# Kernel tuning notes

Hardware: AMD Instinct MI355X
Metric: run time of the kernel (lower is better)

The kernel has to match this reference:

```python
import jax, jax.numpy as jnp
import numpy as np

THETA = 0.5
NEG_SLOPE = 0.2


def setup_inputs() -> dict:
    key = jax.random.key(0)
    k1, k2, k3, k4, k5 = jax.random.split(key, 5)
    B, N, K, E, F = 32, 50000, 32, 6, 3
    return {
        "x": jax.random.normal(k1, (B, N), dtype=jnp.float32),
        "node_embeddings": jax.random.normal(k2, (N, E), dtype=jnp.float32),
        "fc_weight": jax.random.normal(k3, (F, E), dtype=jnp.float32),
        "fc_bias": jax.random.normal(k4, (F,), dtype=jnp.float32),
        "neighbor_list": jax.random.randint(k5, (N, K), 0, N, dtype=jnp.int32),
    }


def reference(x, node_embeddings, fc_weight, fc_bias, neighbor_list):
    # e: (B, N, E) = broadcast-add of scalar feature x and node embeddings
    e = x[..., None] + node_embeddings[None, :, :]
    # f: (B, N, F) = LeakyReLU(e @ W^T + b)
    f = jax.nn.leaky_relu(jnp.einsum('bne,fe->bnf', e, fc_weight) + fc_bias,
                          negative_slope=NEG_SLOPE)
    # gather neighbor features: (B, N, K, F); negative indices wrap like torch
    f_nbr = f[:, neighbor_list]
    df = f[:, :, None, :] - f_nbr               # (B, N, K, F)
    w = jnp.exp(-(df * df).sum(-1) / (2.0 * THETA)).mean(0)  # (N, K)
    mask = (neighbor_list >= 0).astype(w.dtype)
    return w * mask
```

## Files before the change

### kernel.cpp

```cpp
#include <hip/hip_runtime.h>

#define NN 50000
#define BB 32
#define KK 32
#define TN 64
#define GN 8

typedef __attribute__((ext_vector_type(2))) _Float16 half2_t;
typedef __attribute__((ext_vector_type(4))) _Float16 half4_t;
typedef __attribute__((ext_vector_type(8))) _Float16 half8_t;

__device__ __forceinline__ half4_t g_dup0(half8_t v) {
    return __builtin_shufflevector(v, v, 0, 1, 0, 1);
}
__device__ __forceinline__ half4_t g_dup1(half8_t v) {
    return __builtin_shufflevector(v, v, 2, 3, 2, 3);
}
__device__ __forceinline__ half4_t g_dup2(half8_t v) {
    return __builtin_shufflevector(v, v, 4, 5, 4, 5);
}

__global__ __launch_bounds__(256) void prep_kernel(
    const float* __restrict__ x,
    const float* __restrict__ emb,
    const float* __restrict__ W,
    const float* __restrict__ bias,
    half2_t* __restrict__ xT,
    half8_t* __restrict__ gh)
{
    __shared__ float xs[BB][TN + 1];

    const int n0 = blockIdx.x * TN;
    const int t  = threadIdx.x;

#pragma unroll
    for (int j = 0; j < 8; ++j) {
        int idx = j * 256 + t;
        int r = idx >> 6, c = idx & 63;
        int n = n0 + c;
        xs[r][c] = (n < NN) ? x[r * NN + n] : 0.f;
    }
    __syncthreads();

#pragma unroll
    for (int it = 0; it < 4; ++it) {
        int slot = it * 256 + t;
        int nl = slot >> 4, b2 = slot & 15;
        int n = n0 + nl;
        if (n < NN) {
            half2_t p;
            p.x = (_Float16)xs[2 * b2][nl];
            p.y = (_Float16)xs[2 * b2 + 1][nl];
            xT[n * 16 + b2] = p;
            if (b2 == 0) {
                float e[6];
#pragma unroll
                for (int q = 0; q < 6; ++q) e[q] = emb[n * 6 + q];
                half8_t gv;
#pragma unroll
                for (int j = 0; j < 3; ++j) {
                    float s = bias[j];
#pragma unroll
                    for (int q = 0; q < 6; ++q) s += e[q] * W[j * 6 + q];
                    gv[2 * j] = (_Float16)s;
                    gv[2 * j + 1] = (_Float16)s;
                }
                gv[6] = (_Float16)0.f; gv[7] = (_Float16)0.f;
                gh[n] = gv;
            }
        }
    }
}

__global__ __launch_bounds__(256) void gather_kernel(
    const half4_t* __restrict__ xT4,
    const half8_t* __restrict__ gh,
    const float* __restrict__ W,
    const int* __restrict__ nbr,
    float* __restrict__ out)
{
    __shared__ int nbr_sh[GN * KK];

    const int t  = threadIdx.x;
    const int n0 = blockIdx.x * GN;

    nbr_sh[t] = nbr[n0 * KK + t];
    __syncthreads();

    half4_t ws4[3];
#pragma unroll
    for (int j = 0; j < 3; ++j) {
        float s = 0.f;
#pragma unroll
        for (int q = 0; q < 6; ++q) s += W[j * 6 + q];
        _Float16 h = (_Float16)s;
        ws4[j].x = h; ws4[j].y = h; ws4[j].z = h; ws4[j].w = h;
    }
    half4_t lk;
    lk.x = (_Float16)0.2f; lk.y = (_Float16)0.2f;
    lk.z = (_Float16)0.2f; lk.w = (_Float16)0.2f;

    const int l  = t & 7;
    const int sg = t >> 3;
    const int nl = sg >> 2;
    const int kg = (sg & 3) * 8;
    const int n  = n0 + nl;

    half4_t xn4 = xT4[n * 8 + l];
    half8_t gn8 = gh[n];
    half4_t fn[3];
    {
        half4_t u0 = xn4 * ws4[0] + g_dup0(gn8);
        fn[0] = __builtin_elementwise_max(u0, u0 * lk);
        half4_t u1 = xn4 * ws4[1] + g_dup1(gn8);
        fn[1] = __builtin_elementwise_max(u1, u1 * lk);
        half4_t u2 = xn4 * ws4[2] + g_dup2(gn8);
        fn[2] = __builtin_elementwise_max(u2, u2 * lk);
    }

    const int mbase = nl * KK + kg;

#pragma unroll
    for (int i = 0; i < 8; ++i) {
        int m  = nbr_sh[mbase + i];
        int mc = m > 0 ? m : 0;
        half4_t xm4 = xT4[mc * 8 + l];
        half8_t gm8 = gh[mc];

        half4_t acc;
        acc.x = (_Float16)0.f; acc.y = (_Float16)0.f;
        acc.z = (_Float16)0.f; acc.w = (_Float16)0.f;
        {
            half4_t u, d;
            u = xm4 * ws4[0] + g_dup0(gm8);
            u = __builtin_elementwise_max(u, u * lk);
            d = fn[0] - u; acc = d * d + acc;
            u = xm4 * ws4[1] + g_dup1(gm8);
            u = __builtin_elementwise_max(u, u * lk);
            d = fn[1] - u; acc = d * d + acc;
            u = xm4 * ws4[2] + g_dup2(gm8);
            u = __builtin_elementwise_max(u, u * lk);
            d = fn[2] - u; acc = d * d + acc;
        }
        float v = (__expf(-(float)acc.x) + __expf(-(float)acc.y))
                + (__expf(-(float)acc.z) + __expf(-(float)acc.w));
        v += __shfl_down(v, 4, 8);
        v += __shfl_down(v, 2, 8);
        v += __shfl_down(v, 1, 8);
        if (l == 0) out[n * KK + kg + i] = (m < 0) ? 0.f : v * (1.0f / 32.0f);
    }
}

extern "C" void kernel_launch(void* const* d_in, const int* in_sizes, int n_in,
                              void* d_out, int out_size, void* d_ws, size_t ws_size,
                              hipStream_t stream) {
    const float* x    = (const float*)d_in[0];
    const float* emb  = (const float*)d_in[1];
    const float* W    = (const float*)d_in[2];
    const float* bias = (const float*)d_in[3];
    const int*   nbr  = (const int*)d_in[4];
    float* out = (float*)d_out;

    half2_t* xT = (half2_t*)d_ws;
    half8_t* gh = (half8_t*)((char*)d_ws + NN * 16 * sizeof(half2_t));

    prep_kernel<<<(NN + TN - 1) / TN, 256, 0, stream>>>(x, emb, W, bias, xT, gh);
    gather_kernel<<<NN / GN, 256, 0, stream>>>((const half4_t*)xT, gh, W, nbr, out);
}
```

Baseline: 99.26 us.

## Widen gather lanes to half8, fold exp scale into weights, use exp2f

```diff
diff --git a/kernel.cpp b/kernel.cpp
--- a/kernel.cpp
+++ b/kernel.cpp
@@ -1,4 +1,5 @@
 #include <hip/hip_runtime.h>
+#include <math.h>
 
 #define NN 50000
 #define BB 32
@@ -6,18 +7,26 @@
 #define TN 64
 #define GN 8
 
+#define SCL 1.2011224087864498f
+
 typedef __attribute__((ext_vector_type(2))) _Float16 half2_t;
-typedef __attribute__((ext_vector_type(4))) _Float16 half4_t;
 typedef __attribute__((ext_vector_type(8))) _Float16 half8_t;
 
-__device__ __forceinline__ half4_t g_dup0(half8_t v) {
-    return __builtin_shufflevector(v, v, 0, 1, 0, 1);
+__device__ __forceinline__ half8_t dup0(half8_t v) {
+    return __builtin_shufflevector(v, v, 0, 1, 0, 1, 0, 1, 0, 1);
 }
-__device__ __forceinline__ half4_t g_dup1(half8_t v) {
-    return __builtin_shufflevector(v, v, 2, 3, 2, 3);
+__device__ __forceinline__ half8_t dup1(half8_t v) {
+    return __builtin_shufflevector(v, v, 2, 3, 2, 3, 2, 3, 2, 3);
 }
-__device__ __forceinline__ half4_t g_dup2(half8_t v) {
-    return __builtin_shufflevector(v, v, 4, 5, 4, 5);
+__device__ __forceinline__ half8_t dup2(half8_t v) {
+    return __builtin_shufflevector(v, v, 4, 5, 4, 5, 4, 5, 4, 5);
+}
+__device__ __forceinline__ half8_t splat8(float f) {
+    _Float16 h = (_Float16)f;
+    half8_t r;
+    r[0] = h; r[1] = h; r[2] = h; r[3] = h;
+    r[4] = h; r[5] = h; r[6] = h; r[7] = h;
+    return r;
 }
 
 __global__ __launch_bounds__(256) void prep_kernel(
@@ -62,6 +71,7 @@
                     float s = bias[j];
 #pragma unroll
                     for (int q = 0; q < 6; ++q) s += e[q] * W[j * 6 + q];
+                    s *= SCL;
                     gv[2 * j] = (_Float16)s;
                     gv[2 * j + 1] = (_Float16)s;
                 }
@@ -73,7 +83,7 @@
 }
 
 __global__ __launch_bounds__(256) void gather_kernel(
-    const half4_t* __restrict__ xT4,
+    const half8_t* __restrict__ xT8,
     const half8_t* __restrict__ gh,
     const float* __restrict__ W,
     const int* __restrict__ nbr,
@@ -87,67 +97,61 @@
     nbr_sh[t] = nbr[n0 * KK + t];
     __syncthreads();
 
-    half4_t ws4[3];
+    half8_t ws8[3];
 #pragma unroll
     for (int j = 0; j < 3; ++j) {
         float s = 0.f;
 #pragma unroll
         for (int q = 0; q < 6; ++q) s += W[j * 6 + q];
-        _Float16 h = (_Float16)s;
-        ws4[j].x = h; ws4[j].y = h; ws4[j].z = h; ws4[j].w = h;
+        ws8[j] = splat8(s * SCL);
     }
-    half4_t lk;
-    lk.x = (_Float16)0.2f; lk.y = (_Float16)0.2f;
-    lk.z = (_Float16)0.2f; lk.w = (_Float16)0.2f;
+    const half8_t lk = splat8(0.2f);
 
-    const int l  = t & 7;
-    const int sg = t >> 3;
-    const int nl = sg >> 2;
-    const int kg = (sg & 3) * 8;
+    const int l  = t & 3;
+    const int sg = t >> 2;
+    const int nl = sg >> 3;
+    const int kb = (sg & 7) * 4;
     const int n  = n0 + nl;
 
-    half4_t xn4 = xT4[n * 8 + l];
+    half8_t xn8 = xT8[n * 4 + l];
     half8_t gn8 = gh[n];
-    half4_t fn[3];
+    half8_t fn0, fn1, fn2;
     {
-        half4_t u0 = xn4 * ws4[0] + g_dup0(gn8);
-        fn[0] = __builtin_elementwise_max(u0, u0 * lk);
-        half4_t u1 = xn4 * ws4[1] + g_dup1(gn8);
-        fn[1] = __builtin_elementwise_max(u1, u1 * lk);
-        half4_t u2 = xn4 * ws4[2] + g_dup2(gn8);
-        fn[2] = __builtin_elementwise_max(u2, u2 * lk);
+        half8_t u;
+        u = xn8 * ws8[0] + dup0(gn8); fn0 = __builtin_elementwise_max(u, u * lk);
+        u = xn8 * ws8[1] + dup1(gn8); fn1 = __builtin_elementwise_max(u, u * lk);
+        u = xn8 * ws8[2] + dup2(gn8); fn2 = __builtin_elementwise_max(u, u * lk);
     }
 
-    const int mbase = nl * KK + kg;
+    const int mb = nl * KK + kb;
 
 #pragma unroll
-    for (int i = 0; i < 8; ++i) {
-        int m  = nbr_sh[mbase + i];
+    for (int i = 0; i < 4; ++i) {
+        int m  = nbr_sh[mb + i];
         int mc = m > 0 ? m : 0;
-        half4_t xm4 = xT4[mc * 8 + l];
+        half8_t xm8 = xT8[mc * 4 + l];
         half8_t gm8 = gh[mc];
 
-        half4_t acc;
-        acc.x = (_Float16)0.f; acc.y = (_Float16)0.f;
-        acc.z = (_Float16)0.f; acc.w = (_Float16)0.f;
+        half8_t acc = splat8(0.f);
         {
-            half4_t u, d;
-            u = xm4 * ws4[0] + g_dup0(gm8);
+            half8_t u, d;
+            u = xm8 * ws8[0] + dup0(gm8);
             u = __builtin_elementwise_max(u, u * lk);
-            d = fn[0] - u; acc = d * d + acc;
-            u = xm4 * ws4[1] + g_dup1(gm8);
+            d = fn0 - u; acc = d * d + acc;
+            u = xm8 * ws8[1] + dup1(gm8);
             u = __builtin_elementwise_max(u, u * lk);
-            d = fn[1] - u; acc = d * d + acc;
-            u = xm4 * ws4[2] + g_dup2(gm8);
+            d = fn1 - u; acc = d * d + acc;
+            u = xm8 * ws8[2] + dup2(gm8);
             u = __builtin_elementwise_max(u, u * lk);
-            d = fn[2] - u; acc = d * d + acc;
+            d = fn2 - u; acc = d * d + acc;
         }
-        float v = (__expf(-(float)acc.x) + __expf(-(float)acc.y))
-                + (__expf(-(float)acc.z) + __expf(-(float)acc.w));
-        v += __shfl_down(v, 4, 8);
-        v += __shfl_down(v, 2, 8);
-        v += __shfl_down(v, 1, 8);
-        if (l == 0) out[n * KK + kg + i] = (m < 0) ? 0.f : v * (1.0f / 32.0f);
+        float v = (exp2f(-(float)acc[0]) + exp2f(-(float)acc[1]))
+                + (exp2f(-(float)acc[2]) + exp2f(-(float)acc[3]))
+                + (exp2f(-(float)acc[4]) + exp2f(-(float)acc[5]))
+                + (exp2f(-(float)acc[6]) + exp2f(-(float)acc[7]));
+        v += __shfl_down(v, 2, 4);
+        v += __shfl_down(v, 1, 4);
+        if (l == 0) out[n * KK + kb + i] = (m < 0) ? 0.f : v * (1.0f / 32.0f);
     }
 }
 
@@ -165,5 +169,5 @@
     half8_t* gh = (half8_t*)((char*)d_ws + NN * 16 * sizeof(half2_t));
 
     prep_kernel<<<(NN + TN - 1) / TN, 256, 0, stream>>>(x, emb, W, bias, xT, gh);
-    gather_kernel<<<NN / GN, 256, 0, stream>>>((const half4_t*)xT, gh, W, nbr, out);
+    gather_kernel<<<NN / GN, 256, 0, stream>>>((const half8_t*)xT, gh, W, nbr, out);
 }
```

Result: no change. 101.2 us (+1.9%).

## Quantize x to 12-bit and pack per-node row into one 64-byte record

Applied to the files above, without the earlier changes.

```diff
diff --git a/kernel.cpp b/kernel.cpp
--- a/kernel.cpp
+++ b/kernel.cpp
@@ -1,4 +1,5 @@
 #include <hip/hip_runtime.h>
+#include <math.h>
 
 #define NN 50000
 #define BB 32
@@ -6,18 +7,40 @@
 #define TN 64
 #define GN 8
 
+#define SCL 1.2011224087864498f
+#define S0  (4096.0f / 12.0f)
+
 typedef __attribute__((ext_vector_type(2))) _Float16 half2_t;
 typedef __attribute__((ext_vector_type(4))) _Float16 half4_t;
-typedef __attribute__((ext_vector_type(8))) _Float16 half8_t;
-
-__device__ __forceinline__ half4_t g_dup0(half8_t v) {
-    return __builtin_shufflevector(v, v, 0, 1, 0, 1);
-}
-__device__ __forceinline__ half4_t g_dup1(half8_t v) {
-    return __builtin_shufflevector(v, v, 2, 3, 2, 3);
-}
-__device__ __forceinline__ half4_t g_dup2(half8_t v) {
-    return __builtin_shufflevector(v, v, 4, 5, 4, 5);
+
+
+__device__ __forceinline__ half2_t dupc(half4_t v, int which) {
+    if (which == 0) return __builtin_shufflevector(v, v, 0, 0);
+    if (which == 1) return __builtin_shufflevector(v, v, 1, 1);
+    return __builtin_shufflevector(v, v, 2, 2);
+}
+
+__device__ __forceinline__ half2_t pk2(float a, float b) {
+#if __has_builtin(__builtin_amdgcn_cvt_pkrtz)
+    return __builtin_bit_cast(half2_t, __builtin_amdgcn_cvt_pkrtz(a, b));
+#else
+    half2_t r; r.x = (_Float16)a; r.y = (_Float16)b; return r;
+#endif
+}
+
+__device__ __forceinline__ void unpack4(unsigned int lod, unsigned int hiw,
+                                        float K1, float K2,
+                                        half2_t& p01, half2_t& p23) {
+    unsigned int q0 = (lod & 0xFFu)         | ((hiw & 0x000Fu) << 8);
+    unsigned int q1 = ((lod >> 8) & 0xFFu)  | ((hiw & 0x00F0u) << 4);
+    unsigned int q2 = ((lod >> 16) & 0xFFu) | (((hiw >> 8) & 0xFu) << 8);
+    unsigned int q3 = (lod >> 24)           | (((hiw >> 12) & 0xFu) << 8);
+    float p0 = fmaf(__uint_as_float(0x46000000u | q0), K1, K2);
+    float p1 = fmaf(__uint_as_float(0x46000000u | q1), K1, K2);
+    float p2 = fmaf(__uint_as_float(0x46000000u | q2), K1, K2);
+    float p3 = fmaf(__uint_as_float(0x46000000u | q3), K1, K2);
+    p01 = pk2(p0, p1);
+    p23 = pk2(p2, p3);
 }
 
 __global__ __launch_bounds__(256) void prep_kernel(
@@ -25,10 +48,11 @@
     const float* __restrict__ emb,
     const float* __restrict__ W,
     const float* __restrict__ bias,
-    half2_t* __restrict__ xT,
-    half8_t* __restrict__ gh)
+    unsigned int* __restrict__ rows)
 {
     __shared__ float xs[BB][TN + 1];
+    __shared__ unsigned short qs[TN][BB];
+    __shared__ unsigned int ch[TN][2];
 
     const int n0 = blockIdx.x * TN;
     const int t  = threadIdx.x;
@@ -46,35 +70,61 @@
     for (int it = 0; it < 4; ++it) {
         int slot = it * 256 + t;
         int nl = slot >> 4, b2 = slot & 15;
+        int q0 = (int)rintf(xs[2 * b2][nl] * S0) + 2048;
+        int q1 = (int)rintf(xs[2 * b2 + 1][nl] * S0) + 2048;
+        q0 = q0 < 0 ? 0 : (q0 > 4095 ? 4095 : q0);
+        q1 = q1 < 0 ? 0 : (q1 > 4095 ? 4095 : q1);
+        qs[nl][2 * b2]     = (unsigned short)q0;
+        qs[nl][2 * b2 + 1] = (unsigned short)q1;
         int n = n0 + nl;
-        if (n < NN) {
-            half2_t p;
-            p.x = (_Float16)xs[2 * b2][nl];
-            p.y = (_Float16)xs[2 * b2 + 1][nl];
-            xT[n * 16 + b2] = p;
-            if (b2 == 0) {
-                float e[6];
-#pragma unroll
-                for (int q = 0; q < 6; ++q) e[q] = emb[n * 6 + q];
-                half8_t gv;
-#pragma unroll
-                for (int j = 0; j < 3; ++j) {
-                    float s = bias[j];
-#pragma unroll
-                    for (int q = 0; q < 6; ++q) s += e[q] * W[j * 6 + q];
-                    gv[2 * j] = (_Float16)s;
-                    gv[2 * j + 1] = (_Float16)s;
-                }
-                gv[6] = (_Float16)0.f; gv[7] = (_Float16)0.f;
-                gh[n] = gv;
+        if (b2 == 0 && n < NN) {
+            float e[6];
+#pragma unroll
+            for (int q = 0; q < 6; ++q) e[q] = emb[n * 6 + q];
+            unsigned short cb[3];
+#pragma unroll
+            for (int j = 0; j < 3; ++j) {
+                float s = bias[j];
+#pragma unroll
+                for (int q = 0; q < 6; ++q) s += e[q] * W[j * 6 + q];
+                _Float16 h = (_Float16)(s * SCL);
+                cb[j] = __builtin_bit_cast(unsigned short, h);
             }
-        }
+            ch[nl][0] = (unsigned int)cb[0] | ((unsigned int)cb[1] << 16);
+            ch[nl][1] = (unsigned int)cb[2];
+        }
+    }
+    __syncthreads();
+
+#pragma unroll
+    for (int it = 0; it < 4; ++it) {
+        int slot = it * 256 + t;
+        int nl = slot >> 4, d = slot & 15;
+        int n = n0 + nl;
+        if (n >= NN) continue;
+        unsigned int w = 0;
+        if (d < 8) {
+            int b = 4 * d;
+            w = ((unsigned int)(qs[nl][b] & 0xFF))
+              | ((unsigned int)(qs[nl][b + 1] & 0xFF) << 8)
+              | ((unsigned int)(qs[nl][b + 2] & 0xFF) << 16)
+              | ((unsigned int)(qs[nl][b + 3] & 0xFF) << 24);
+        } else if (d < 12) {
+            int i0 = 8 * (d - 8);
+#pragma unroll
+            for (int i = 0; i < 8; ++i)
+                w |= ((unsigned int)(qs[nl][i0 + i] >> 8)) << (4 * i);
+        } else if (d == 12) {
+            w = ch[nl][0];
+        } else if (d == 13) {
+            w = ch[nl][1];
+        }
+        rows[(size_t)n * 16 + d] = w;
     }
 }
 
 __global__ __launch_bounds__(256) void gather_kernel(
-    const half4_t* __restrict__ xT4,
-    const half8_t* __restrict__ gh,
+    const unsigned int* __restrict__ rows,
     const float* __restrict__ W,
     const int* __restrict__ nbr,
     float* __restrict__ out)
@@ -83,71 +133,82 @@
 
     const int t  = threadIdx.x;
     const int n0 = blockIdx.x * GN;
+    const unsigned short* rows16 = (const unsigned short*)rows;
 
     nbr_sh[t] = nbr[n0 * KK + t];
     __syncthreads();
 
-    half4_t ws4[3];
+    const float K1 = 1024.0f * SCL / S0;
+    const float K2 = -8390656.0f * SCL / S0;
+
+    half2_t wsh[3];
 #pragma unroll
     for (int j = 0; j < 3; ++j) {
         float s = 0.f;
 #pragma unroll
         for (int q = 0; q < 6; ++q) s += W[j * 6 + q];
         _Float16 h = (_Float16)s;
-        ws4[j].x = h; ws4[j].y = h; ws4[j].z = h; ws4[j].w = h;
-    }
-    half4_t lk;
-    lk.x = (_Float16)0.2f; lk.y = (_Float16)0.2f;
-    lk.z = (_Float16)0.2f; lk.w = (_Float16)0.2f;
+        wsh[j].x = h; wsh[j].y = h;
+    }
+    half2_t lk; lk.x = (_Float16)0.2f; lk.y = (_Float16)0.2f;
 
     const int l  = t & 7;
     const int sg = t >> 3;
     const int nl = sg >> 2;
-    const int kg = (sg & 3) * 8;
+    const int kb = (sg & 3) * 8;
     const int n  = n0 + nl;
 
-    half4_t xn4 = xT4[n * 8 + l];
-    half8_t gn8 = gh[n];
-    half4_t fn[3];
+    half2_t fn01[3], fn23[3];
     {
-        half4_t u0 = xn4 * ws4[0] + g_dup0(gn8);
-        fn[0] = __builtin_elementwise_max(u0, u0 * lk);
-        half4_t u1 = xn4 * ws4[1] + g_dup1(gn8);
-        fn[1] = __builtin_elementwise_max(u1, u1 * lk);
-        half4_t u2 = xn4 * ws4[2] + g_dup2(gn8);
-        fn[2] = __builtin_elementwise_max(u2, u2 * lk);
-    }
-
-    const int mbase = nl * KK + kg;
+        unsigned int lod = rows[(size_t)n * 16 + l];
+        unsigned short hiw = rows16[(size_t)n * 32 + 16 + l];
+        half4_t c4 = *(const half4_t*)(rows + (size_t)n * 16 + 12);
+        half2_t p01, p23;
+        unpack4(lod, hiw, K1, K2, p01, p23);
+#pragma unroll
+        for (int j = 0; j < 3; ++j) {
+            half2_t g = dupc(c4, j);
+            half2_t u = p01 * wsh[j] + g;
+            fn01[j] = __builtin_elementwise_max(u, u * lk);
+            u = p23 * wsh[j] + g;
+            fn23[j] = __builtin_elementwise_max(u, u * lk);
+        }
+    }
+
+    const int mb = nl * KK + kb;
 
 #pragma unroll
     for (int i = 0; i < 8; ++i) {
-        int m  = nbr_sh[mbase + i];
+        int m  = nbr_sh[mb + i];
         int mc = m > 0 ? m : 0;
-        half4_t xm4 = xT4[mc * 8 + l];
-        half8_t gm8 = gh[mc];
-
-        half4_t acc;
-        acc.x = (_Float16)0.f; acc.y = (_Float16)0.f;
-        acc.z = (_Float16)0.f; acc.w = (_Float16)0.f;
-        {
-            half4_t u, d;
-            u = xm4 * ws4[0] + g_dup0(gm8);
+        unsigned int lod = rows[(size_t)mc * 16 + l];
+        unsigned short hiw = rows16[(size_t)mc * 32 + 16 + l];
+        half4_t c4 = *(const half4_t*)(rows + (size_t)mc * 16 + 12);
+
+        half2_t p01, p23;
+        unpack4(lod, hiw, K1, K2, p01, p23);
+
+        half2_t a01, a23;
+        a01.x = (_Float16)0.f; a01.y = (_Float16)0.f;
+        a23 = a01;
+#pragma unroll
+        for (int j = 0; j < 3; ++j) {
+            half2_t g = dupc(c4, j);
+            half2_t u = p01 * wsh[j] + g;
             u = __builtin_elementwise_max(u, u * lk);
-            d = fn[0] - u; acc = d * d + acc;
-            u = xm4 * ws4[1] + g_dup1(gm8);
+            half2_t d = fn01[j] - u;
+            a01 = d * d + a01;
+            u = p23 * wsh[j] + g;
             u = __builtin_elementwise_max(u, u * lk);
-            d = fn[1] - u; acc = d * d + acc;
-            u = xm4 * ws4[2] + g_dup2(gm8);
-            u = __builtin_elementwise_max(u, u * lk);
-            d = fn[2] - u; acc = d * d + acc;
-        }
-        float v = (__expf(-(float)acc.x) + __expf(-(float)acc.y))
-                + (__expf(-(float)acc.z) + __expf(-(float)acc.w));
+            d = fn23[j] - u;
+            a23 = d * d + a23;
+        }
+        float v = (exp2f(-(float)a01.x) + exp2f(-(float)a01.y))
+                + (exp2f(-(float)a23.x) + exp2f(-(float)a23.y));
         v += __shfl_down(v, 4, 8);
         v += __shfl_down(v, 2, 8);
         v += __shfl_down(v, 1, 8);
-        if (l == 0) out[n * KK + kg + i] = (m < 0) ? 0.f : v * (1.0f / 32.0f);
+        if (l == 0) out[n * KK + kb + i] = (m < 0) ? 0.f : v * (1.0f / 32.0f);
     }
 }
 
@@ -161,9 +222,8 @@
     const int*   nbr  = (const int*)d_in[4];
     float* out = (float*)d_out;
 
-    half2_t* xT = (half2_t*)d_ws;
-    half8_t* gh = (half8_t*)((char*)d_ws + NN * 16 * sizeof(half2_t));
-
-    prep_kernel<<<(NN + TN - 1) / TN, 256, 0, stream>>>(x, emb, W, bias, xT, gh);
-    gather_kernel<<<NN / GN, 256, 0, stream>>>((const half4_t*)xT, gh, W, nbr, out);
-}
+    unsigned int* rows = (unsigned int*)d_ws;
+
+    prep_kernel<<<(NN + TN - 1) / TN, 256, 0, stream>>>(x, emb, W, bias, rows);
+    gather_kernel<<<NN / GN, 256, 0, stream>>>(rows, W, nbr, out);
+}
```

New measurement: 105.3 us. 1.06x slower.
